# Optimization experiments

Measured on AMD Instinct MI355X. Metric: run time of the kernel, lower is better.

Reference implementation:

```python
import jax, jax.numpy as jnp
import numpy as np

# Dims: tokens [B,H,W,C]; 3x3 local window (NB=9 neighbors); relative-pos embed dim RP.
B, H, W, C = 4, 96, 96, 128
K, NB, RP = 3, 9, 8
HID = 128              # edge_hidden_dim = max(hidden_dim//2=128, feature_dim=128)
EDGE_IN = 3 * C + RP   # [center, neighbor, center-neighbor, rel_pos] -> 392
CLIP = 3.0
GATE_EPS = 1e-6
LN_EPS = 1e-5


def _ln(x, w, b):
    m = jnp.mean(x, axis=-1, keepdims=True)
    v = jnp.mean((x - m) ** 2, axis=-1, keepdims=True)
    return (x - m) * jax.lax.rsqrt(v + LN_EPS) * w + b


def _mlp(x, w1, b1, w2, b2):
    # Linear -> GELU (exact/erf, torch default) -> Linear; dropout is identity in eval mode.
    return jax.nn.gelu(x @ w1 + b1, approximate=False) @ w2 + b2


def _eml(drive, resistance, gamma_raw, lam, bias, warmup_eta):
    # EMLUnit energy gate (source not provided; Ohm's-law style drive/resistance,
    # positive resistance via softplus, clipped, warmup-scaled, learned bias).
    gamma = jax.nn.softplus(gamma_raw)
    conduct = drive / (jax.nn.softplus(resistance) + gamma + GATE_EPS)
    return warmup_eta * jnp.clip(lam * conduct, -CLIP, CLIP) + bias


def setup_inputs() -> dict:
    key = jax.random.key(0)
    ks = jax.random.split(key, 8)

    def w(k, shape, std=0.01):
        return jax.random.normal(k, shape, jnp.float32) * std

    return {
        "tokens": jax.random.normal(ks[0], (B, H, W, C), jnp.float32),
        "ln1_w": jnp.ones((C,), jnp.float32), "ln1_b": jnp.zeros((C,), jnp.float32),
        "ln2_w": jnp.ones((C,), jnp.float32), "ln2_b": jnp.zeros((C,), jnp.float32),
        "rel_pos": w(ks[1], (NB, RP), 0.02),
        "d_w1": w(ks[2], (EDGE_IN, HID)), "d_b1": jnp.zeros((HID,), jnp.float32),
        "d_w2": w(ks[3], (HID, 1)), "d_b2": jnp.zeros((1,), jnp.float32),
        "r_w1": w(ks[4], (EDGE_IN, HID)), "r_b1": jnp.zeros((HID,), jnp.float32),
        "r_w2": w(ks[5], (HID, 1)), "r_b2": jnp.zeros((1,), jnp.float32),
        "v_w": w(ks[6], (C, C)), "v_b": jnp.zeros((C,), jnp.float32),
        "o_w": w(ks[7], (C, C)), "o_b": jnp.zeros((C,), jnp.float32),
        "eml_gamma": jnp.full((1,), 0.1, jnp.float32),
        "eml_lam": jnp.ones((1,), jnp.float32),
        "eml_bias": jnp.full((1,), -0.3, jnp.float32),
    }


def reference(tokens, ln1_w, ln1_b, ln2_w, ln2_b, rel_pos,
              d_w1, d_b1, d_w2, d_b2, r_w1, r_b1, r_w2, r_b2,
              v_w, v_b, o_w, o_b, eml_gamma, eml_lam, eml_bias):
    b, h, w_, c = tokens.shape
    hw = h * w_
    norm = _ln(tokens, ln1_w, ln1_b)
    # nn.Unfold(kernel=3, padding=1): zero-pad then gather 3x3 windows (row-major ky,kx order).
    pad = jnp.pad(norm, ((0, 0), (1, 1), (1, 1), (0, 0)))
    neigh = jnp.stack([pad[:, dy:dy + h, dx:dx + w_, :]
                       for dy in range(K) for dx in range(K)], axis=3)  # [B,H,W,9,C]
    neigh = neigh.reshape(b, hw, NB, c)
    center = jnp.broadcast_to(norm.reshape(b, hw, 1, c), (b, hw, NB, c))
    relp = jnp.broadcast_to(rel_pos[None, None], (b, hw, NB, RP))
    edge = jnp.concatenate([center, neigh, center - neigh, relp], axis=-1)  # [B,HW,9,392]
    drive = _mlp(edge, d_w1, d_b1, d_w2, d_b2)[..., 0]        # [B,HW,9]
    resistance = _mlp(edge, r_w1, r_b1, r_w2, r_b2)[..., 0]   # [B,HW,9]
    energy = _eml(drive, resistance, eml_gamma, eml_lam, eml_bias, 1.0)
    gate = jax.nn.sigmoid(energy)[..., None]                  # [B,HW,9,1]
    values = neigh @ v_w + v_b                                # [B,HW,9,C]
    gate_mass = jnp.clip(jnp.sum(gate, axis=2), GATE_EPS, None)  # [B,HW,1]
    message = jnp.sum(gate * values, axis=2) / gate_mass      # [B,HW,C]
    update = (message @ o_w + o_b).reshape(b, h, w_, c)
    return _ln(tokens + update, ln2_w, ln2_b)
```

## Files before the change

### kernel.cpp

```cpp
#include <hip/hip_runtime.h>
#include <stdint.h>

#define NPIX 36864

using bf16x8 = __attribute__((ext_vector_type(8))) short;
using f32x4  = __attribute__((ext_vector_type(4))) float;
using f32x2  = __attribute__((ext_vector_type(2))) float;

__device__ __forceinline__ float bf2f(uint16_t u){
  return __uint_as_float(((uint32_t)u) << 16);
}
__device__ __forceinline__ float bl(uint32_t u){ return __uint_as_float(u << 16); }
__device__ __forceinline__ float bh(uint32_t u){ return __uint_as_float(u & 0xFFFF0000u); }
__device__ __forceinline__ uint16_t f2bf(float f){
  uint32_t u = __float_as_uint(f);
  u += 0x7fffu + ((u >> 16) & 1u);
  return (uint16_t)(u >> 16);
}
__device__ __forceinline__ float ldw(const void* p, int i, bool f32){
  return f32 ? ((const float*)p)[i] : bf2f(((const uint16_t*)p)[i]);
}
__device__ __forceinline__ bool probe_f32(const void* ones_vec){
  return ((const uint32_t*)ones_vec)[0] == 0x3F800000u;
}
__device__ __forceinline__ float softplusf(float x){
  return fmaxf(x, 0.f) + __logf(1.f + __expf(-fabsf(x)));
}
__device__ __forceinline__ f32x2 up2(uint32_t u){
  f32x2 r; r.x = __uint_as_float(u << 16); r.y = __uint_as_float(u & 0xFFFF0000u); return r;
}
__device__ __forceinline__ void sg2(f32x2& acc, uint32_t c, uint32_t n, f32x2 r, f32x2 w){
  f32x2 z = up2(c) + up2(n) + r;
  float sx = __builtin_amdgcn_fmed3f(fmaf(z.x, 0.4255f, 0.5f), 0.f, 1.f);
  float sy = __builtin_amdgcn_fmed3f(fmaf(z.y, 0.4255f, 0.5f), 0.f, 1.f);
  acc.x = fmaf(z.x * sx, w.x, acc.x);
  acc.y = fmaf(z.y * sy, w.y, acc.y);
}

#define LIDX(p, ch) ((p)*128 + ((((ch) >> 3) ^ ((p) & 15)) << 3) + ((ch) & 7))

__global__ __launch_bounds__(256) void pre_kernel(const void* __restrict__ tokens,
                            const void* __restrict__ ln1w, const void* __restrict__ ln1b,
                            const void* __restrict__ dw1, const void* __restrict__ rw1,
                            const void* __restrict__ vw,  const void* __restrict__ relp,
                            const void* __restrict__ db1, const void* __restrict__ rb1,
                            const void* __restrict__ ow,
                            const void* __restrict__ dw2, const void* __restrict__ rw2,
                            const void* __restrict__ vb,  const void* __restrict__ db2,
                            const void* __restrict__ rb2, const void* __restrict__ eg,
                            const void* __restrict__ el,  const void* __restrict__ eb,
                            uint16_t* __restrict__ norm,
                            uint16_t* __restrict__ wcatT, float* __restrict__ Rd,
                            float* __restrict__ Rr, uint16_t* __restrict__ owT,
                            float* __restrict__ w2df, float* __restrict__ w2rf,
                            float* __restrict__ vbf, float* __restrict__ sc){
  const bool F = probe_f32(ln1w);
  const int b = blockIdx.x;
  if (b < NPIX/4){
    const int wv = threadIdx.x >> 6, lane = threadIdx.x & 63;
    const int p = b * 4 + wv;
    float f0, f1;
    if (F){
      const float2 t = ((const float2*)tokens)[(size_t)p*64 + lane];
      f0 = t.x; f1 = t.y;
    } else {
      const uint32_t pk = ((const uint32_t*)tokens)[(size_t)p*64 + lane];
      f0 = bl(pk); f1 = bh(pk);
    }
    float s = f0 + f1;
    #pragma unroll
    for (int m = 1; m < 64; m <<= 1) s += __shfl_xor(s, m, 64);
    const float mean = s * (1.f/128.f);
    const float d0 = f0 - mean, d1 = f1 - mean;
    float q = d0*d0 + d1*d1;
    #pragma unroll
    for (int m = 1; m < 64; m <<= 1) q += __shfl_xor(q, m, 64);
    const float rs = rsqrtf(q * (1.f/128.f) + 1e-5f);
    const float n0 = d0*rs*ldw(ln1w, 2*lane, F)   + ldw(ln1b, 2*lane, F);
    const float n1 = d1*rs*ldw(ln1w, 2*lane+1, F) + ldw(ln1b, 2*lane+1, F);
    ((uint32_t*)(norm + (size_t)p*128))[lane] = (uint32_t)f2bf(n0) | ((uint32_t)f2bf(n1) << 16);
    return;
  }
  const int j = (b - NPIX/4) * 2 + (threadIdx.x >> 7);
  const int c = threadIdx.x & 127;
  if (j < 640){
    float val;
    if (j < 128)      val = ldw(dw1, c*128 + j, F)             + ldw(dw1, (256+c)*128 + j, F);
    else if (j < 256) val = ldw(dw1, (128+c)*128 + (j-128), F) - ldw(dw1, (256+c)*128 + (j-128), F);
    else if (j < 384) val = ldw(rw1, c*128 + (j-256), F)       + ldw(rw1, (256+c)*128 + (j-256), F);
    else if (j < 512) val = ldw(rw1, (128+c)*128 + (j-384), F) - ldw(rw1, (256+c)*128 + (j-384), F);
    else              val = ldw(vw, c*128 + (j-512), F);
    wcatT[j*128 + c] = f2bf(val);
  } else if (j < 649){
    const int k = j - 640;
    float sd = ldw(db1, c, F);
    float sr = ldw(rb1, c, F);
    #pragma unroll
    for (int r = 0; r < 8; ++r){
      float rp = ldw(relp, k*8 + r, F);
      sd += rp * ldw(dw1, (384+r)*128 + c, F);
      sr += rp * ldw(rw1, (384+r)*128 + c, F);
    }
    Rd[k*128 + c] = sd;
    Rr[k*128 + c] = sr;
  } else if (j < 777){
    const int n = j - 649;
    owT[n*128 + c] = f2bf(ldw(ow, c*128 + n, F));
  } else {
    w2df[c] = ldw(dw2, c, F);
    w2rf[c] = ldw(rw2, c, F);
    vbf[c]  = ldw(vb, c, F);
    if (c == 0){
      sc[0] = ldw(db2, 0, F);
      sc[1] = ldw(rb2, 0, F);
      sc[2] = softplusf(ldw(eg, 0, F));
      sc[3] = ldw(el, 0, F);
      sc[4] = ldw(eb, 0, F);
    }
  }
}

__global__ __launch_bounds__(256) void gemm1_kernel(const uint16_t* __restrict__ A,
                                                    const uint16_t* __restrict__ BT,
                                                    uint16_t* __restrict__ PT,
                                                    uint16_t* __restrict__ V){
  __shared__ __align__(16) char smem[49152];
  uint16_t* As = (uint16_t*)smem;
  uint16_t* Bs = (uint16_t*)(smem + 16384);
  const int row0 = blockIdx.x * 64;
  const int s    = blockIdx.y;
  const int t = threadIdx.x;
  #pragma unroll
  for (int i = 0; i < 4; ++i){
    const int cid = t + i*256;
    const int r = cid >> 4, c8 = cid & 15;
    *(uint4*)&As[r*128 + ((c8 ^ (r & 15)) << 3)] = *(const uint4*)&A[(size_t)(row0+r)*128 + c8*8];
  }
  #pragma unroll
  for (int i = 0; i < 8; ++i){
    const int cid = t + i*256;
    const int r = cid >> 4, c8 = cid & 15;
    *(uint4*)&Bs[r*128 + ((c8 ^ (r & 15)) << 3)] = *(const uint4*)&BT[(size_t)(s*128 + r)*128 + c8*8];
  }
  __syncthreads();
  const int wv = t >> 6, lane = t & 63;
  const int wc = wv * 32;
  const int lr = lane & 15, quad = lane >> 4;
  f32x4 acc[4][2] = {};
  #pragma unroll
  for (int kk = 0; kk < 4; ++kk){
    const int chunk = kk*4 + quad;
    bf16x8 a[4], b[2];
    #pragma unroll
    for (int mi = 0; mi < 4; ++mi){
      const int r = mi*16 + lr;
      a[mi] = *(const bf16x8*)&As[r*128 + ((chunk ^ (r & 15)) << 3)];
    }
    #pragma unroll
    for (int ni = 0; ni < 2; ++ni){
      const int r = wc + ni*16 + lr;
      b[ni] = *(const bf16x8*)&Bs[r*128 + ((chunk ^ (r & 15)) << 3)];
    }
    #pragma unroll
    for (int mi = 0; mi < 4; ++mi)
      #pragma unroll
      for (int ni = 0; ni < 2; ++ni)
        acc[mi][ni] = __builtin_amdgcn_mfma_f32_16x16x32_bf16(a[mi], b[ni], acc[mi][ni], 0, 0, 0);
  }
  __syncthreads();
  #pragma unroll
  for (int mi = 0; mi < 4; ++mi){
    #pragma unroll
    for (int ni = 0; ni < 2; ++ni){
      const int ch   = wc + ni*16 + lr;
      const int rowb = mi*16 + quad*4;
      #pragma unroll
      for (int r = 0; r < 4; ++r)
        As[LIDX(rowb + r, ch)] = f2bf(acc[mi][ni][r]);
    }
  }
  __syncthreads();
  if (s < 4){
    #pragma unroll
    for (int i = 0; i < 4; ++i){
      const int idx = t + i*256;
      const int p = idx & 63, c = idx >> 6;
      const uint4 v = *(const uint4*)&As[p*128 + ((c ^ (p & 15)) << 3)];
      ((uint4*)PT)[(size_t)(s*16 + c)*NPIX + (row0 + p)] = v;
    }
  } else {
    #pragma unroll
    for (int i = 0; i < 4; ++i){
      const int idx = t + i*256;
      const int c8 = idx & 15, p = idx >> 4;
      const uint4 v = *(const uint4*)&As[p*128 + ((c8 ^ (p & 15)) << 3)];
      ((uint4*)V)[(size_t)(row0 + p)*16 + c8] = v;
    }
  }
}

__global__ __launch_bounds__(64) void edge_kernel(const uint16_t* __restrict__ PTraw,
    const float* __restrict__ Rd, const float* __restrict__ Rr,
    const float* __restrict__ w2df, const float* __restrict__ w2rf,
    const float* __restrict__ sc, float* __restrict__ gates){
  const int lane = threadIdx.x;
  const int k = blockIdx.y;
  const int p = blockIdx.x * 64 + lane;
  const int dy = k/3 - 1, dx = k%3 - 1;
  const int x = p % 96, y = (p / 96) % 96;
  const bool inb = ((unsigned)(x + dx) < 96u) && ((unsigned)(y + dy) < 96u);
  const uint32_t m = inb ? 0xFFFFFFFFu : 0u;
  const int q = inb ? (p + dy*96 + dx) : p;
  const uint4* Cp = (const uint4*)PTraw + p;
  const uint4* Np = (const uint4*)PTraw + q;
  const float sc0 = sc[0], sc1 = sc[1], sc2 = sc[2], sc3 = sc[3], sc4 = sc[4];

  f32x2 ad = {0.f, 0.f};
  {
    const float4* r4 = (const float4*)(Rd + k*128);
    const float4* w4 = (const float4*)w2df;
    uint4 c = Cp[0];
    uint4 n = Np[(size_t)16*NPIX];
    #pragma unroll
    for (int i = 0; i < 16; ++i){
      uint4 cn, nn;
      if (i < 15){
        cn = Cp[(size_t)(i+1)*NPIX];
        nn = Np[(size_t)(16 + i+1)*NPIX];
      }
      n.x &= m; n.y &= m; n.z &= m; n.w &= m;
      const float4 rA = r4[2*i], rB = r4[2*i+1];
      const float4 wA = w4[2*i], wB = w4[2*i+1];
      sg2(ad, c.x, n.x, f32x2{rA.x, rA.y}, f32x2{wA.x, wA.y});
      sg2(ad, c.y, n.y, f32x2{rA.z, rA.w}, f32x2{wA.z, wA.w});
      sg2(ad, c.z, n.z, f32x2{rB.x, rB.y}, f32x2{wB.x, wB.y});
      sg2(ad, c.w, n.w, f32x2{rB.z, rB.w}, f32x2{wB.z, wB.w});
      c = cn; n = nn;
    }
  }
  f32x2 ar = {0.f, 0.f};
  {
    const float4* r4 = (const float4*)(Rr + k*128);
    const float4* w4 = (const float4*)w2rf;
    uint4 c = Cp[(size_t)32*NPIX];
    uint4 n = Np[(size_t)48*NPIX];
    #pragma unroll
    for (int i = 0; i < 16; ++i){
      uint4 cn, nn;
      if (i < 15){
        cn = Cp[(size_t)(32 + i+1)*NPIX];
        nn = Np[(size_t)(48 + i+1)*NPIX];
      }
      n.x &= m; n.y &= m; n.z &= m; n.w &= m;
      const float4 rA = r4[2*i], rB = r4[2*i+1];
      const float4 wA = w4[2*i], wB = w4[2*i+1];
      sg2(ar, c.x, n.x, f32x2{rA.x, rA.y}, f32x2{wA.x, wA.y});
      sg2(ar, c.y, n.y, f32x2{rA.z, rA.w}, f32x2{wA.z, wA.w});
      sg2(ar, c.z, n.z, f32x2{rB.x, rB.y}, f32x2{wB.x, wB.y});
      sg2(ar, c.w, n.w, f32x2{rB.z, rB.w}, f32x2{wB.z, wB.w});
      c = cn; n = nn;
    }
  }
  const float drive  = (ad.x + ad.y) + sc0;
  const float resist = (ar.x + ar.y) + sc1;
  const float cond = __fdividef(drive, softplusf(resist) + sc2 + 1e-6f);
  const float en = fminf(fmaxf(sc3 * cond, -3.0f), 3.0f) + sc4;
  const float e = __expf(-en);
  const float g = __builtin_amdgcn_rcpf(1.0f + e);
  gates[(size_t)k*NPIX + p] = g;
}

__global__ __launch_bounds__(256) void msg_kernel(const uint16_t* __restrict__ V,
    const float* __restrict__ gates, const float* __restrict__ vbf,
    uint16_t* __restrict__ msg){
  const int wv = __builtin_amdgcn_readfirstlane(threadIdx.x >> 6);
  const int lane = threadIdx.x & 63;
  const int p = blockIdx.x * 4 + wv;
  const int x = p % 96, y = (p / 96) % 96;
  float g[9], gsum = 0.f;
  #pragma unroll
  for (int k = 0; k < 9; ++k){ g[k] = gates[(size_t)k*NPIX + p]; gsum += g[k]; }
  float a0 = 0.f, a1 = 0.f;
  #pragma unroll
  for (int k = 0; k < 9; ++k){
    const int dy = k/3 - 1, dx = k%3 - 1;
    if (((unsigned)(y + dy) < 96u) && ((unsigned)(x + dx) < 96u)){
      const uint32_t u = ((const uint32_t*)(V + (size_t)(p + dy*96 + dx)*128))[lane];
      a0 = fmaf(g[k], bl(u), a0);
      a1 = fmaf(g[k], bh(u), a1);
    }
  }
  const float2 vb2 = ((const float2*)vbf)[lane];
  const float inv = __fdividef(1.0f, fmaxf(gsum, 1e-6f));
  a0 = (a0 + gsum * vb2.x) * inv;
  a1 = (a1 + gsum * vb2.y) * inv;
  ((uint32_t*)(msg + (size_t)p*128))[lane] = (uint32_t)f2bf(a0) | ((uint32_t)f2bf(a1) << 16);
}

__global__ __launch_bounds__(256) void out_kernel(const uint16_t* __restrict__ Amsg,
    const uint16_t* __restrict__ owT, const void* __restrict__ tokens,
    const void* __restrict__ ob,  const void* __restrict__ ln2w,
    const void* __restrict__ ln2b, void* __restrict__ out){
  const bool F = probe_f32(ln2w);
  __shared__ __align__(16) char smem[49152];
  uint16_t* Bs = (uint16_t*)smem;
  uint16_t* As = (uint16_t*)(smem + 32768);
  float*    U  = (float*)smem;
  const int row0 = blockIdx.x * 64;
  const int t = threadIdx.x;
  const int wv = t >> 6, lane = t & 63;
  #pragma unroll
  for (int i = 0; i < 8; ++i){
    const int cid = t + i*256;
    const int r = cid >> 4, c8 = cid & 15;
    *(uint4*)&Bs[r*128 + ((c8 ^ (r & 15)) << 3)] = *(const uint4*)&owT[(size_t)r*128 + c8*8];
  }
  #pragma unroll
  for (int i = 0; i < 4; ++i){
    const int cid = t + i*256;
    const int r = cid >> 4, c8 = cid & 15;
    *(uint4*)&As[r*128 + ((c8 ^ (r & 15)) << 3)] = *(const uint4*)&Amsg[(size_t)(row0+r)*128 + c8*8];
  }
  __syncthreads();
  const int wc = wv * 32;
  const int lr = lane & 15, quad = lane >> 4;
  f32x4 acc[4][2] = {};
  #pragma unroll
  for (int kk = 0; kk < 4; ++kk){
    const int chunk = kk*4 + quad;
    bf16x8 a[4], b[2];
    #pragma unroll
    for (int mi = 0; mi < 4; ++mi){
      const int r = mi*16 + lr;
      a[mi] = *(const bf16x8*)&As[r*128 + ((chunk ^ (r & 15)) << 3)];
    }
    #pragma unroll
    for (int ni = 0; ni < 2; ++ni){
      const int r = wc + ni*16 + lr;
      b[ni] = *(const bf16x8*)&Bs[r*128 + ((chunk ^ (r & 15)) << 3)];
    }
    #pragma unroll
    for (int mi = 0; mi < 4; ++mi)
      #pragma unroll
      for (int ni = 0; ni < 2; ++ni)
        acc[mi][ni] = __builtin_amdgcn_mfma_f32_16x16x32_bf16(a[mi], b[ni], acc[mi][ni], 0, 0, 0);
  }
  __syncthreads();
  #pragma unroll
  for (int mi = 0; mi < 4; ++mi)
    #pragma unroll
    for (int ni = 0; ni < 2; ++ni)
      #pragma unroll
      for (int r = 0; r < 4; ++r)
        U[(mi*16 + quad*4 + r)*128 + wc + ni*16 + lr] = acc[mi][ni][r];
  __syncthreads();
  const float lw0 = ldw(ln2w, 2*lane, F), lw1 = ldw(ln2w, 2*lane+1, F);
  const float lb0 = ldw(ln2b, 2*lane, F), lb1 = ldw(ln2b, 2*lane+1, F);
  const float ob0 = ldw(ob, 2*lane, F),   ob1 = ldw(ob, 2*lane+1, F);
  for (int j = 0; j < 16; ++j){
    const int row = wv*16 + j;
    const int p = row0 + row;
    const float2 uv = ((const float2*)U)[row*64 + lane];
    float t0, t1;
    if (F){
      const float2 tk = ((const float2*)tokens)[(size_t)p*64 + lane];
      t0 = tk.x; t1 = tk.y;
    } else {
      const uint32_t tk = ((const uint32_t*)tokens)[(size_t)p*64 + lane];
      t0 = bl(tk); t1 = bh(tk);
    }
    const float a0 = uv.x + ob0 + t0;
    const float a1 = uv.y + ob1 + t1;
    float s = a0 + a1;
    #pragma unroll
    for (int m = 1; m < 64; m <<= 1) s += __shfl_xor(s, m, 64);
    const float mean = s * (1.f/128.f);
    const float d0 = a0 - mean, d1 = a1 - mean;
    float q = d0*d0 + d1*d1;
    #pragma unroll
    for (int m = 1; m < 64; m <<= 1) q += __shfl_xor(q, m, 64);
    const float rs = rsqrtf(q * (1.f/128.f) + 1e-5f);
    const float o0 = d0*rs*lw0 + lb0;
    const float o1 = d1*rs*lw1 + lb1;
    if (F){
      ((float2*)out)[(size_t)p*64 + lane] = make_float2(o0, o1);
    } else {
      ((uint32_t*)out)[(size_t)p*64 + lane] = (uint32_t)f2bf(o0) | ((uint32_t)f2bf(o1) << 16);
    }
  }
}

extern "C" void kernel_launch(void* const* d_in, const int* in_sizes, int n_in,
                              void* d_out, int out_size, void* d_ws, size_t ws_size,
                              hipStream_t stream) {
  const void* tokens = d_in[0];
  const void* ln1w   = d_in[1];
  const void* ln1b   = d_in[2];
  const void* ln2w   = d_in[3];
  const void* ln2b   = d_in[4];
  const void* relp   = d_in[5];
  const void* dw1    = d_in[6];
  const void* db1    = d_in[7];
  const void* dw2    = d_in[8];
  const void* db2    = d_in[9];
  const void* rw1    = d_in[10];
  const void* rb1    = d_in[11];
  const void* rw2    = d_in[12];
  const void* rb2    = d_in[13];
  const void* vw     = d_in[14];
  const void* vb     = d_in[15];
  const void* ow     = d_in[16];
  const void* ob     = d_in[17];
  const void* eg     = d_in[18];
  const void* el     = d_in[19];
  const void* eb     = d_in[20];

  char* ws = (char*)d_ws;
  uint16_t* normb = (uint16_t*)(ws + 0);
  uint16_t* PT    = (uint16_t*)(ws + 9437184);
  uint16_t* V     = (uint16_t*)(ws + 47185920);
  float*    gates = (float*)   (ws + 56623104);
  uint16_t* wcatT = (uint16_t*)(ws + 57950208);
  float*    Rd    = (float*)   (ws + 58114048);
  float*    Rr    = (float*)   (ws + 58118656);
  uint16_t* owT   = (uint16_t*)(ws + 58123264);
  float*    w2df  = (float*)   (ws + 58156032);
  float*    w2rf  = (float*)   (ws + 58156544);
  float*    vbf   = (float*)   (ws + 58157056);
  float*    sc    = (float*)   (ws + 58157568);
  uint16_t* msg   = normb;

  pre_kernel<<<NPIX/4 + 389, 256, 0, stream>>>(tokens, ln1w, ln1b,
                                       dw1, rw1, vw, relp, db1, rb1, ow,
                                       dw2, rw2, vb, db2, rb2, eg, el, eb,
                                       normb, wcatT, Rd, Rr, owT, w2df, w2rf, vbf, sc);
  gemm1_kernel<<<dim3(NPIX/64, 5), 256, 0, stream>>>(normb, wcatT, PT, V);
  edge_kernel<<<dim3(NPIX/64, 9), 64, 0, stream>>>(PT, Rd, Rr, w2df, w2rf, sc, gates);
  msg_kernel<<<NPIX/4, 256, 0, stream>>>(V, gates, vbf, msg);
  out_kernel<<<NPIX/64, 256, 0, stream>>>(msg, owT, tokens, ob, ln2w, ln2b, d_out);
}
```

Measured before the change: 200.8 us.

## Fuse edge gating and message aggregation into one tiled kernel with LDS halo

Merges the edge and message kernels into a single kernel that works on 8x8 spatial tiles. Each block stages the neighbor projections and values, plus a one-pixel halo, in shared memory, so neighbor data is reused across the nine offsets instead of being re-read from global memory. Gates stay in LDS rather than going through a global buffer. The gemm1 output layout for PT changes from channel-major to pixel-major to suit this. The cost is a large LDS footprint (~79KB) with 576-thread blocks, which limits occupancy, and only 576 blocks are launched.

```diff
diff --git a/kernel.cpp b/kernel.cpp
--- a/kernel.cpp
+++ b/kernel.cpp
@@ -180,55 +180,87 @@
     }
   }
   __syncthreads();
-  if (s < 4){
-    #pragma unroll
-    for (int i = 0; i < 4; ++i){
-      const int idx = t + i*256;
-      const int p = idx & 63, c = idx >> 6;
-      const uint4 v = *(const uint4*)&As[p*128 + ((c ^ (p & 15)) << 3)];
-      ((uint4*)PT)[(size_t)(s*16 + c)*NPIX + (row0 + p)] = v;
-    }
-  } else {
-    #pragma unroll
-    for (int i = 0; i < 4; ++i){
-      const int idx = t + i*256;
-      const int c8 = idx & 15, p = idx >> 4;
-      const uint4 v = *(const uint4*)&As[p*128 + ((c8 ^ (p & 15)) << 3)];
-      ((uint4*)V)[(size_t)(row0 + p)*16 + c8] = v;
-    }
-  }
-}
-
-__global__ __launch_bounds__(64) void edge_kernel(const uint16_t* __restrict__ PTraw,
+  uint16_t* const dst = (s == 4) ? V : (PT + (size_t)s * NPIX * 128);
+  #pragma unroll
+  for (int i = 0; i < 4; ++i){
+    const int idx = t + i*256;
+    const int c8 = idx & 15, p = idx >> 4;
+    const uint4 v = *(const uint4*)&As[p*128 + ((c8 ^ (p & 15)) << 3)];
+    ((uint4*)dst)[(size_t)(row0 + p)*16 + c8] = v;
+  }
+}
+
+__global__ __launch_bounds__(576) void emsg_kernel(
+    const uint16_t* __restrict__ PT, const uint16_t* __restrict__ Vg,
     const float* __restrict__ Rd, const float* __restrict__ Rr,
     const float* __restrict__ w2df, const float* __restrict__ w2rf,
-    const float* __restrict__ sc, float* __restrict__ gates){
-  const int lane = threadIdx.x;
-  const int k = blockIdx.y;
-  const int p = blockIdx.x * 64 + lane;
-  const int dy = k/3 - 1, dx = k%3 - 1;
-  const int x = p % 96, y = (p / 96) % 96;
-  const bool inb = ((unsigned)(x + dx) < 96u) && ((unsigned)(y + dy) < 96u);
-  const uint32_t m = inb ? 0xFFFFFFFFu : 0u;
-  const int q = inb ? (p + dy*96 + dx) : p;
-  const uint4* Cp = (const uint4*)PTraw + p;
-  const uint4* Np = (const uint4*)PTraw + q;
+    const float* __restrict__ sc, const float* __restrict__ vbf,
+    uint16_t* __restrict__ msg){
+  __shared__ __align__(16) char smem[79104];
+  uint16_t* const PnD = (uint16_t*)smem;
+  uint16_t* const PnR = (uint16_t*)(smem + 25600);
+  uint16_t* const Vl  = (uint16_t*)(smem + 51200);
+  float*    const gl  = (float*)  (smem + 76800);
+
+  const int bid = blockIdx.x;
+  const int b   = bid / 144;
+  const int tl  = bid - b*144;
+  const int ty  = tl / 12;
+  const int y0  = ty * 8;
+  const int x0  = (tl - ty*12) * 8;
+  const int tid = threadIdx.x;
+
+  const uint16_t* const P1 = PT + (size_t)NPIX*128;
+  const uint16_t* const P3 = PT + (size_t)3*NPIX*128;
+
+  for (int i = tid; i < 4800; i += 576){
+    const int arr = i / 1600;
+    const int rem = i - arr*1600;
+    const int hq  = rem >> 4;
+    const int ch  = rem & 15;
+    const int hy  = hq / 10;
+    const int hx  = hq - hy*10;
+    const int y = y0 - 1 + hy, x = x0 - 1 + hx;
+    uint4 v = {0u, 0u, 0u, 0u};
+    if (((unsigned)y < 96u) && ((unsigned)x < 96u)){
+      const size_t pg = (size_t)((b*96 + y)*96 + x);
+      const uint16_t* src = (arr == 0 ? P1 : (arr == 1 ? P3 : Vg)) + pg*128 + ch*8;
+      v = *(const uint4*)src;
+    }
+    if (arr == 2){
+      *(uint4*)&Vl[hq*128 + ch*8] = v;
+    } else {
+      uint16_t* const d = (arr == 0) ? PnD : PnR;
+      *(uint4*)((char*)d + hq*256 + ((ch ^ (hq & 15)) << 4)) = v;
+    }
+  }
+  __syncthreads();
+
+  const int wv = tid >> 6, lane = tid & 63;
+  const int k  = __builtin_amdgcn_readfirstlane(wv);
+  const int ky = k / 3, kx = k - ky*3;
+  const int py = lane >> 3, px = lane & 7;
+  const int hq = (py + ky)*10 + (px + kx);
+  const size_t pg = (size_t)((b*96 + y0 + py)*96 + (x0 + px));
   const float sc0 = sc[0], sc1 = sc[1], sc2 = sc[2], sc3 = sc[3], sc4 = sc[4];
+  const char* const nbD = (const char*)PnD + hq*256;
+  const char* const nbR = (const char*)PnR + hq*256;
+  const int hsw = hq & 15;
 
   f32x2 ad = {0.f, 0.f};
   {
+    const uint4*  Cp = (const uint4*)(PT + pg*128);
     const float4* r4 = (const float4*)(Rd + k*128);
     const float4* w4 = (const float4*)w2df;
     uint4 c = Cp[0];
-    uint4 n = Np[(size_t)16*NPIX];
+    uint4 n = *(const uint4*)(nbD + ((0 ^ hsw) << 4));
     #pragma unroll
     for (int i = 0; i < 16; ++i){
       uint4 cn, nn;
       if (i < 15){
-        cn = Cp[(size_t)(i+1)*NPIX];
-        nn = Np[(size_t)(16 + i+1)*NPIX];
+        cn = Cp[i+1];
+        nn = *(const uint4*)(nbD + (((i+1) ^ hsw) << 4));
       }
-      n.x &= m; n.y &= m; n.z &= m; n.w &= m;
       const float4 rA = r4[2*i], rB = r4[2*i+1];
       const float4 wA = w4[2*i], wB = w4[2*i+1];
       sg2(ad, c.x, n.x, f32x2{rA.x, rA.y}, f32x2{wA.x, wA.y});
@@ -240,18 +272,18 @@
   }
   f32x2 ar = {0.f, 0.f};
   {
+    const uint4*  Cp = (const uint4*)(PT + (size_t)2*NPIX*128 + pg*128);
     const float4* r4 = (const float4*)(Rr + k*128);
     const float4* w4 = (const float4*)w2rf;
-    uint4 c = Cp[(size_t)32*NPIX];
-    uint4 n = Np[(size_t)48*NPIX];
+    uint4 c = Cp[0];
+    uint4 n = *(const uint4*)(nbR + ((0 ^ hsw) << 4));
     #pragma unroll
     for (int i = 0; i < 16; ++i){
       uint4 cn, nn;
       if (i < 15){
-        cn = Cp[(size_t)(32 + i+1)*NPIX];
-        nn = Np[(size_t)(48 + i+1)*NPIX];
+        cn = Cp[i+1];
+        nn = *(const uint4*)(nbR + (((i+1) ^ hsw) << 4));
       }
-      n.x &= m; n.y &= m; n.z &= m; n.w &= m;
       const float4 rA = r4[2*i], rB = r4[2*i+1];
       const float4 wA = w4[2*i], wB = w4[2*i+1];
       sg2(ar, c.x, n.x, f32x2{rA.x, rA.y}, f32x2{wA.x, wA.y});
@@ -266,35 +298,34 @@
   const float cond = __fdividef(drive, softplusf(resist) + sc2 + 1e-6f);
   const float en = fminf(fmaxf(sc3 * cond, -3.0f), 3.0f) + sc4;
   const float e = __expf(-en);
-  const float g = __builtin_amdgcn_rcpf(1.0f + e);
-  gates[(size_t)k*NPIX + p] = g;
-}
-
-__global__ __launch_bounds__(256) void msg_kernel(const uint16_t* __restrict__ V,
-    const float* __restrict__ gates, const float* __restrict__ vbf,
-    uint16_t* __restrict__ msg){
-  const int wv = __builtin_amdgcn_readfirstlane(threadIdx.x >> 6);
-  const int lane = threadIdx.x & 63;
-  const int p = blockIdx.x * 4 + wv;
-  const int x = p % 96, y = (p / 96) % 96;
-  float g[9], gsum = 0.f;
-  #pragma unroll
-  for (int k = 0; k < 9; ++k){ g[k] = gates[(size_t)k*NPIX + p]; gsum += g[k]; }
-  float a0 = 0.f, a1 = 0.f;
-  #pragma unroll
-  for (int k = 0; k < 9; ++k){
-    const int dy = k/3 - 1, dx = k%3 - 1;
-    if (((unsigned)(y + dy) < 96u) && ((unsigned)(x + dx) < 96u)){
-      const uint32_t u = ((const uint32_t*)(V + (size_t)(p + dy*96 + dx)*128))[lane];
-      a0 = fmaf(g[k], bl(u), a0);
-      a1 = fmaf(g[k], bh(u), a1);
-    }
-  }
-  const float2 vb2 = ((const float2*)vbf)[lane];
-  const float inv = __fdividef(1.0f, fmaxf(gsum, 1e-6f));
-  a0 = (a0 + gsum * vb2.x) * inv;
-  a1 = (a1 + gsum * vb2.y) * inv;
-  ((uint32_t*)(msg + (size_t)p*128))[lane] = (uint32_t)f2bf(a0) | ((uint32_t)f2bf(a1) << 16);
+  gl[k*64 + lane] = __builtin_amdgcn_rcpf(1.0f + e);
+  __syncthreads();
+
+  if (wv < 8){
+    const float2 vb2 = ((const float2*)vbf)[lane];
+    #pragma unroll
+    for (int j = 0; j < 8; ++j){
+      const int m  = wv*8 + j;
+      const int my = m >> 3, mx = m & 7;
+      float gk[9], gsum = 0.f;
+      #pragma unroll
+      for (int kk = 0; kk < 9; ++kk){ gk[kk] = gl[kk*64 + m]; gsum += gk[kk]; }
+      float a0 = 0.f, a1 = 0.f;
+      #pragma unroll
+      for (int kk = 0; kk < 9; ++kk){
+        const int kyy = kk / 3;
+        const int h2  = (my + kyy)*10 + (mx + kk - kyy*3);
+        const uint32_t u = ((const uint32_t*)Vl)[h2*64 + lane];
+        a0 = fmaf(gk[kk], bl(u), a0);
+        a1 = fmaf(gk[kk], bh(u), a1);
+      }
+      const float inv = __fdividef(1.0f, fmaxf(gsum, 1e-6f));
+      a0 = (a0 + gsum * vb2.x) * inv;
+      a1 = (a1 + gsum * vb2.y) * inv;
+      const size_t p2 = (size_t)((b*96 + y0 + my)*96 + (x0 + mx));
+      ((uint32_t*)msg)[p2*64 + lane] = (uint32_t)f2bf(a0) | ((uint32_t)f2bf(a1) << 16);
+    }
+  }
 }
 
 __global__ __launch_bounds__(256) void out_kernel(const uint16_t* __restrict__ Amsg,
@@ -419,7 +450,6 @@
   uint16_t* normb = (uint16_t*)(ws + 0);
   uint16_t* PT    = (uint16_t*)(ws + 9437184);
   uint16_t* V     = (uint16_t*)(ws + 47185920);
-  float*    gates = (float*)   (ws + 56623104);
   uint16_t* wcatT = (uint16_t*)(ws + 57950208);
   float*    Rd    = (float*)   (ws + 58114048);
   float*    Rr    = (float*)   (ws + 58118656);
@@ -435,7 +465,6 @@
                                        dw2, rw2, vb, db2, rb2, eg, el, eb,
                                        normb, wcatT, Rd, Rr, owT, w2df, w2rf, vbf, sc);
   gemm1_kernel<<<dim3(NPIX/64, 5), 256, 0, stream>>>(normb, wcatT, PT, V);
-  edge_kernel<<<dim3(NPIX/64, 9), 64, 0, stream>>>(PT, Rd, Rr, w2df, w2rf, sc, gates);
-  msg_kernel<<<NPIX/4, 256, 0, stream>>>(V, gates, vbf, msg);
+  emsg_kernel<<<576, 576, 0, stream>>>(PT, V, Rd, Rr, w2df, w2rf, sc, vbf, msg);
   out_kernel<<<NPIX/64, 256, 0, stream>>>(msg, owT, tokens, ob, ln2w, ln2b, d_out);
 }
```

Result: faster. 193.8 us (-3.5%).

## Fuse gemm, edge, message and output stages into one tiled mega kernel

Applied to the files above, without the earlier changes.

Replaces four kernels (projection GEMM, edge gating, gated message aggregation, output GEMM+LayerNorm) with one kernel per 8x8 spatial tile. Each tile stages a 10x10 halo of normalized tokens in LDS and recomputes the per-neighbor projections on that halo. Projections, gates and messages then stay in shared memory instead of round-tripping large intermediates (PT, V, gates, msg) through global memory. The cost is redundant halo GEMM work, heavy LDS usage (~108KB) limiting occupancy to one block per CU, many block-wide barriers, and only 576 blocks.

```diff
diff --git a/kernel.cpp b/kernel.cpp
--- a/kernel.cpp
+++ b/kernel.cpp
@@ -120,253 +120,239 @@
   }
 }
 
-__global__ __launch_bounds__(256) void gemm1_kernel(const uint16_t* __restrict__ A,
-                                                    const uint16_t* __restrict__ BT,
-                                                    uint16_t* __restrict__ PT,
-                                                    uint16_t* __restrict__ V){
-  __shared__ __align__(16) char smem[49152];
-  uint16_t* As = (uint16_t*)smem;
-  uint16_t* Bs = (uint16_t*)(smem + 16384);
-  const int row0 = blockIdx.x * 64;
-  const int s    = blockIdx.y;
-  const int t = threadIdx.x;
+__global__ __launch_bounds__(512) void mega_kernel(
+    const uint16_t* __restrict__ norm, const uint16_t* __restrict__ wcatT,
+    const uint16_t* __restrict__ owT,
+    const float* __restrict__ Rd, const float* __restrict__ Rr,
+    const float* __restrict__ w2df, const float* __restrict__ w2rf,
+    const float* __restrict__ sc, const float* __restrict__ vbf,
+    const void* __restrict__ tokens, const void* __restrict__ ob,
+    const void* __restrict__ ln2w, const void* __restrict__ ln2b,
+    void* __restrict__ out){
+  __shared__ __align__(16) char smem[111104];
+  uint16_t* const Ns = (uint16_t*)smem;
+  uint16_t* const PA = (uint16_t*)(smem + 28672);
+  uint16_t* const PB = (uint16_t*)(smem + 57344);
+  uint16_t* const Ws = (uint16_t*)(smem + 73728);
+  float*    const drv = (float*)(smem + 106496);
+  float*    const gts = (float*)(smem + 108800);
+  float*    const U   = (float*)smem;
+
+  const int bid0 = blockIdx.x;
+  const int bid  = (bid0 & 7)*72 + (bid0 >> 3);
+  const int b  = bid / 144;
+  const int tl = bid - b*144;
+  const int ty = tl / 12;
+  const int y0 = ty*8, x0 = (tl - ty*12)*8;
+  const int tid = threadIdx.x;
+  const int wv = tid >> 6, lane = tid & 63;
+  const int lr = lane & 15, quad = lane >> 4;
+  const float sc0 = sc[0], sc1 = sc[1], sc2 = sc[2], sc3 = sc[3], sc4 = sc[4];
+
   #pragma unroll
   for (int i = 0; i < 4; ++i){
-    const int cid = t + i*256;
-    const int r = cid >> 4, c8 = cid & 15;
-    *(uint4*)&As[r*128 + ((c8 ^ (r & 15)) << 3)] = *(const uint4*)&A[(size_t)(row0+r)*128 + c8*8];
-  }
-  #pragma unroll
-  for (int i = 0; i < 8; ++i){
-    const int cid = t + i*256;
-    const int r = cid >> 4, c8 = cid & 15;
-    *(uint4*)&Bs[r*128 + ((c8 ^ (r & 15)) << 3)] = *(const uint4*)&BT[(size_t)(s*128 + r)*128 + c8*8];
-  }
+    const int idx = tid + i*512;
+    if (idx < 1792){
+      const int hq = idx >> 4, g = idx & 15;
+      uint4 v = {0u,0u,0u,0u};
+      if (hq < 100){
+        const int hy = hq/10, hx = hq - hy*10;
+        const int y = y0 - 1 + hy, x = x0 - 1 + hx;
+        if (((unsigned)y < 96u) && ((unsigned)x < 96u))
+          v = *(const uint4*)&norm[((size_t)((b*96+y)*96+x))*128 + g*8];
+      }
+      *(uint4*)&Ns[hq*128 + ((g ^ (hq & 15)) << 3)] = v;
+    }
+  }
+
+  auto stageW = [&](const uint16_t* __restrict__ src){
+    #pragma unroll
+    for (int i = 0; i < 4; ++i){
+      const int idx = tid + i*512;
+      const int r = idx >> 4, g = idx & 15;
+      *(uint4*)&Ws[r*128 + ((g ^ (r & 15)) << 3)] = *(const uint4*)&src[(size_t)r*128 + g*8];
+    }
+  };
+
+  auto gemmH = [&](){
+    f32x4 acc[7] = {};
+    #pragma unroll
+    for (int kk = 0; kk < 4; ++kk){
+      const int chunk = kk*4 + quad;
+      const bf16x8 bf = *(const bf16x8*)&Ws[(wv*16+lr)*128 + ((chunk ^ lr) << 3)];
+      #pragma unroll
+      for (int mi = 0; mi < 7; ++mi){
+        const int r = mi*16 + lr;
+        const bf16x8 a = *(const bf16x8*)&Ns[r*128 + ((chunk ^ (r & 15)) << 3)];
+        acc[mi] = __builtin_amdgcn_mfma_f32_16x16x32_bf16(a, bf, acc[mi], 0, 0, 0);
+      }
+    }
+    const int col = wv*16 + lr;
+    #pragma unroll
+    for (int mi = 0; mi < 7; ++mi){
+      const int rowb = mi*16 + quad*4;
+      #pragma unroll
+      for (int r = 0; r < 4; ++r)
+        PA[LIDX(rowb + r, col)] = f2bf(acc[mi][r]);
+    }
+  };
+
+  auto gemmC = [&](){
+    f32x4 acc[4] = {};
+    #pragma unroll
+    for (int kk = 0; kk < 4; ++kk){
+      const int chunk = kk*4 + quad;
+      const bf16x8 bf = *(const bf16x8*)&Ws[(wv*16+lr)*128 + ((chunk ^ lr) << 3)];
+      #pragma unroll
+      for (int mi = 0; mi < 4; ++mi){
+        const int r = mi*16 + lr;
+        const int hr = (r >> 3)*10 + (r & 7) + 11;
+        const bf16x8 a = *(const bf16x8*)&Ns[hr*128 + ((chunk ^ (hr & 15)) << 3)];
+        acc[mi] = __builtin_amdgcn_mfma_f32_16x16x32_bf16(a, bf, acc[mi], 0, 0, 0);
+      }
+    }
+    const int col = wv*16 + lr;
+    #pragma unroll
+    for (int mi = 0; mi < 4; ++mi){
+      const int rowb = mi*16 + quad*4;
+      #pragma unroll
+      for (int r = 0; r < 4; ++r)
+        PB[LIDX(rowb + r, col)] = f2bf(acc[mi][r]);
+    }
+  };
+
+  auto edge = [&](const float* __restrict__ Rk, const float* __restrict__ w2, bool isDrive){
+    const int pl = lane >> 3, cg = lane & 7;
+    for (int i = 0; i < 9; ++i){
+      const int it = wv*9 + i;
+      const int k = it >> 3, ry = it & 7;
+      const int ky = k/3, kx = k - ky*3;
+      const int pr = ry*8 + pl;
+      const int hq = (ry + ky)*10 + pl + kx;
+      const int g0 = 2*cg;
+      const uint4 c0 = *(const uint4*)((const char*)PB + pr*256 + (((g0)  ^ (pr & 15)) << 4));
+      const uint4 c1 = *(const uint4*)((const char*)PB + pr*256 + (((g0+1)^ (pr & 15)) << 4));
+      const uint4 n0 = *(const uint4*)((const char*)PA + hq*256 + (((g0)  ^ (hq & 15)) << 4));
+      const uint4 n1 = *(const uint4*)((const char*)PA + hq*256 + (((g0+1)^ (hq & 15)) << 4));
+      const float4* r4 = (const float4*)(Rk + k*128) + cg*4;
+      const float4* w4 = (const float4*)w2 + cg*4;
+      const float4 Ra = r4[0], Rb = r4[1], Rc = r4[2], Rv = r4[3];
+      const float4 Wa = w4[0], Wb = w4[1], Wc = w4[2], Wd = w4[3];
+      f32x2 a = {0.f, 0.f};
+      sg2(a, c0.x, n0.x, f32x2{Ra.x, Ra.y}, f32x2{Wa.x, Wa.y});
+      sg2(a, c0.y, n0.y, f32x2{Ra.z, Ra.w}, f32x2{Wa.z, Wa.w});
+      sg2(a, c0.z, n0.z, f32x2{Rb.x, Rb.y}, f32x2{Wb.x, Wb.y});
+      sg2(a, c0.w, n0.w, f32x2{Rb.z, Rb.w}, f32x2{Wb.z, Wb.w});
+      sg2(a, c1.x, n1.x, f32x2{Rc.x, Rc.y}, f32x2{Wc.x, Wc.y});
+      sg2(a, c1.y, n1.y, f32x2{Rc.z, Rc.w}, f32x2{Wc.z, Wc.w});
+      sg2(a, c1.z, n1.z, f32x2{Rv.x, Rv.y}, f32x2{Wd.x, Wd.y});
+      sg2(a, c1.w, n1.w, f32x2{Rv.z, Rv.w}, f32x2{Wd.z, Wd.w});
+      float s = a.x + a.y;
+      s += __shfl_xor(s, 1, 64); s += __shfl_xor(s, 2, 64); s += __shfl_xor(s, 4, 64);
+      if (cg == 0){
+        if (isDrive){
+          drv[k*64 + pr] = s;
+        } else {
+          const float drive  = drv[k*64 + pr] + sc0;
+          const float resist = s + sc1;
+          const float cond = __fdividef(drive, softplusf(resist) + sc2 + 1e-6f);
+          const float en = fminf(fmaxf(sc3 * cond, -3.0f), 3.0f) + sc4;
+          const float e = __expf(-en);
+          gts[k*64 + pr] = __builtin_amdgcn_rcpf(1.0f + e);
+        }
+      }
+    }
+  };
+
+  const uint16_t* const W0 = wcatT;
+  const uint16_t* const W1 = wcatT + (size_t)1*128*128;
+  const uint16_t* const W2 = wcatT + (size_t)2*128*128;
+  const uint16_t* const W3 = wcatT + (size_t)3*128*128;
+  const uint16_t* const W4 = wcatT + (size_t)4*128*128;
+
+  stageW(W1); __syncthreads();
+  gemmH();    __syncthreads();
+  stageW(W0); __syncthreads();
+  gemmC();    __syncthreads();
+  stageW(W3);
+  edge(Rd, w2df, true);
   __syncthreads();
-  const int wv = t >> 6, lane = t & 63;
-  const int wc = wv * 32;
-  const int lr = lane & 15, quad = lane >> 4;
-  f32x4 acc[4][2] = {};
+  gemmH();    __syncthreads();
+  stageW(W2); __syncthreads();
+  gemmC();    __syncthreads();
+  stageW(W4);
+  edge(Rr, w2rf, false);
+  __syncthreads();
+  gemmH();    __syncthreads();
+  stageW(owT);
+
+  {
+    const float2 vb2 = ((const float2*)vbf)[lane];
+    const int g = lane >> 2, lb = (lane & 3)*4;
+    #pragma unroll
+    for (int j = 0; j < 8; ++j){
+      const int mp = wv*8 + j;
+      const int my = mp >> 3, mx = mp & 7;
+      float gk[9], gsum = 0.f;
+      #pragma unroll
+      for (int kk = 0; kk < 9; ++kk){ gk[kk] = gts[kk*64 + mp]; gsum += gk[kk]; }
+      float a0 = 0.f, a1 = 0.f;
+      #pragma unroll
+      for (int kk = 0; kk < 9; ++kk){
+        const int kyy = kk / 3;
+        const int h2  = (my + kyy)*10 + (mx + kk - kyy*3);
+        const uint32_t u = *(const uint32_t*)((const char*)PA + h2*256 + ((g ^ (h2 & 15)) << 4) + lb);
+        a0 = fmaf(gk[kk], bl(u), a0);
+        a1 = fmaf(gk[kk], bh(u), a1);
+      }
+      const float inv = __fdividef(1.0f, fmaxf(gsum, 1e-6f));
+      a0 = (a0 + gsum * vb2.x) * inv;
+      a1 = (a1 + gsum * vb2.y) * inv;
+      *(uint32_t*)((char*)PB + mp*256 + ((g ^ (mp & 15)) << 4) + lb) =
+          (uint32_t)f2bf(a0) | ((uint32_t)f2bf(a1) << 16);
+    }
+  }
+  __syncthreads();
+
+  f32x4 acc[4] = {};
   #pragma unroll
   for (int kk = 0; kk < 4; ++kk){
     const int chunk = kk*4 + quad;
-    bf16x8 a[4], b[2];
+    const bf16x8 bf = *(const bf16x8*)&Ws[(wv*16+lr)*128 + ((chunk ^ lr) << 3)];
     #pragma unroll
     for (int mi = 0; mi < 4; ++mi){
       const int r = mi*16 + lr;
-      a[mi] = *(const bf16x8*)&As[r*128 + ((chunk ^ (r & 15)) << 3)];
-    }
-    #pragma unroll
-    for (int ni = 0; ni < 2; ++ni){
-      const int r = wc + ni*16 + lr;
-      b[ni] = *(const bf16x8*)&Bs[r*128 + ((chunk ^ (r & 15)) << 3)];
-    }
+      const bf16x8 a = *(const bf16x8*)&PB[r*128 + ((chunk ^ (r & 15)) << 3)];
+      acc[mi] = __builtin_amdgcn_mfma_f32_16x16x32_bf16(a, bf, acc[mi], 0, 0, 0);
+    }
+  }
+  __syncthreads();
+  {
+    const int col = wv*16 + lr;
     #pragma unroll
     for (int mi = 0; mi < 4; ++mi)
       #pragma unroll
-      for (int ni = 0; ni < 2; ++ni)
-        acc[mi][ni] = __builtin_amdgcn_mfma_f32_16x16x32_bf16(a[mi], b[ni], acc[mi][ni], 0, 0, 0);
+      for (int r = 0; r < 4; ++r)
+        U[(mi*16 + quad*4 + r)*128 + col] = acc[mi][r];
   }
   __syncthreads();
-  #pragma unroll
-  for (int mi = 0; mi < 4; ++mi){
-    #pragma unroll
-    for (int ni = 0; ni < 2; ++ni){
-      const int ch   = wc + ni*16 + lr;
-      const int rowb = mi*16 + quad*4;
-      #pragma unroll
-      for (int r = 0; r < 4; ++r)
-        As[LIDX(rowb + r, ch)] = f2bf(acc[mi][ni][r]);
-    }
-  }
-  __syncthreads();
-  if (s < 4){
-    #pragma unroll
-    for (int i = 0; i < 4; ++i){
-      const int idx = t + i*256;
-      const int p = idx & 63, c = idx >> 6;
-      const uint4 v = *(const uint4*)&As[p*128 + ((c ^ (p & 15)) << 3)];
-      ((uint4*)PT)[(size_t)(s*16 + c)*NPIX + (row0 + p)] = v;
-    }
-  } else {
-    #pragma unroll
-    for (int i = 0; i < 4; ++i){
-      const int idx = t + i*256;
-      const int c8 = idx & 15, p = idx >> 4;
-      const uint4 v = *(const uint4*)&As[p*128 + ((c8 ^ (p & 15)) << 3)];
-      ((uint4*)V)[(size_t)(row0 + p)*16 + c8] = v;
-    }
-  }
-}
-
-__global__ __launch_bounds__(64) void edge_kernel(const uint16_t* __restrict__ PTraw,
-    const float* __restrict__ Rd, const float* __restrict__ Rr,
-    const float* __restrict__ w2df, const float* __restrict__ w2rf,
-    const float* __restrict__ sc, float* __restrict__ gates){
-  const int lane = threadIdx.x;
-  const int k = blockIdx.y;
-  const int p = blockIdx.x * 64 + lane;
-  const int dy = k/3 - 1, dx = k%3 - 1;
-  const int x = p % 96, y = (p / 96) % 96;
-  const bool inb = ((unsigned)(x + dx) < 96u) && ((unsigned)(y + dy) < 96u);
-  const uint32_t m = inb ? 0xFFFFFFFFu : 0u;
-  const int q = inb ? (p + dy*96 + dx) : p;
-  const uint4* Cp = (const uint4*)PTraw + p;
-  const uint4* Np = (const uint4*)PTraw + q;
-  const float sc0 = sc[0], sc1 = sc[1], sc2 = sc[2], sc3 = sc[3], sc4 = sc[4];
-
-  f32x2 ad = {0.f, 0.f};
-  {
-    const float4* r4 = (const float4*)(Rd + k*128);
-    const float4* w4 = (const float4*)w2df;
-    uint4 c = Cp[0];
-    uint4 n = Np[(size_t)16*NPIX];
-    #pragma unroll
-    for (int i = 0; i < 16; ++i){
-      uint4 cn, nn;
-      if (i < 15){
-        cn = Cp[(size_t)(i+1)*NPIX];
-        nn = Np[(size_t)(16 + i+1)*NPIX];
-      }
-      n.x &= m; n.y &= m; n.z &= m; n.w &= m;
-      const float4 rA = r4[2*i], rB = r4[2*i+1];
-      const float4 wA = w4[2*i], wB = w4[2*i+1];
-      sg2(ad, c.x, n.x, f32x2{rA.x, rA.y}, f32x2{wA.x, wA.y});
-      sg2(ad, c.y, n.y, f32x2{rA.z, rA.w}, f32x2{wA.z, wA.w});
-      sg2(ad, c.z, n.z, f32x2{rB.x, rB.y}, f32x2{wB.x, wB.y});
-      sg2(ad, c.w, n.w, f32x2{rB.z, rB.w}, f32x2{wB.z, wB.w});
-      c = cn; n = nn;
-    }
-  }
-  f32x2 ar = {0.f, 0.f};
-  {
-    const float4* r4 = (const float4*)(Rr + k*128);
-    const float4* w4 = (const float4*)w2rf;
-    uint4 c = Cp[(size_t)32*NPIX];
-    uint4 n = Np[(size_t)48*NPIX];
-    #pragma unroll
-    for (int i = 0; i < 16; ++i){
-      uint4 cn, nn;
-      if (i < 15){
-        cn = Cp[(size_t)(32 + i+1)*NPIX];
-        nn = Np[(size_t)(48 + i+1)*NPIX];
-      }
-      n.x &= m; n.y &= m; n.z &= m; n.w &= m;
-      const float4 rA = r4[2*i], rB = r4[2*i+1];
-      const float4 wA = w4[2*i], wB = w4[2*i+1];
-      sg2(ar, c.x, n.x, f32x2{rA.x, rA.y}, f32x2{wA.x, wA.y});
-      sg2(ar, c.y, n.y, f32x2{rA.z, rA.w}, f32x2{wA.z, wA.w});
-      sg2(ar, c.z, n.z, f32x2{rB.x, rB.y}, f32x2{wB.x, wB.y});
-      sg2(ar, c.w, n.w, f32x2{rB.z, rB.w}, f32x2{wB.z, wB.w});
-      c = cn; n = nn;
-    }
-  }
-  const float drive  = (ad.x + ad.y) + sc0;
-  const float resist = (ar.x + ar.y) + sc1;
-  const float cond = __fdividef(drive, softplusf(resist) + sc2 + 1e-6f);
-  const float en = fminf(fmaxf(sc3 * cond, -3.0f), 3.0f) + sc4;
-  const float e = __expf(-en);
-  const float g = __builtin_amdgcn_rcpf(1.0f + e);
-  gates[(size_t)k*NPIX + p] = g;
-}
-
-__global__ __launch_bounds__(256) void msg_kernel(const uint16_t* __restrict__ V,
-    const float* __restrict__ gates, const float* __restrict__ vbf,
-    uint16_t* __restrict__ msg){
-  const int wv = __builtin_amdgcn_readfirstlane(threadIdx.x >> 6);
-  const int lane = threadIdx.x & 63;
-  const int p = blockIdx.x * 4 + wv;
-  const int x = p % 96, y = (p / 96) % 96;
-  float g[9], gsum = 0.f;
-  #pragma unroll
-  for (int k = 0; k < 9; ++k){ g[k] = gates[(size_t)k*NPIX + p]; gsum += g[k]; }
-  float a0 = 0.f, a1 = 0.f;
-  #pragma unroll
-  for (int k = 0; k < 9; ++k){
-    const int dy = k/3 - 1, dx = k%3 - 1;
-    if (((unsigned)(y + dy) < 96u) && ((unsigned)(x + dx) < 96u)){
-      const uint32_t u = ((const uint32_t*)(V + (size_t)(p + dy*96 + dx)*128))[lane];
-      a0 = fmaf(g[k], bl(u), a0);
-      a1 = fmaf(g[k], bh(u), a1);
-    }
-  }
-  const float2 vb2 = ((const float2*)vbf)[lane];
-  const float inv = __fdividef(1.0f, fmaxf(gsum, 1e-6f));
-  a0 = (a0 + gsum * vb2.x) * inv;
-  a1 = (a1 + gsum * vb2.y) * inv;
-  ((uint32_t*)(msg + (size_t)p*128))[lane] = (uint32_t)f2bf(a0) | ((uint32_t)f2bf(a1) << 16);
-}
-
-__global__ __launch_bounds__(256) void out_kernel(const uint16_t* __restrict__ Amsg,
-    const uint16_t* __restrict__ owT, const void* __restrict__ tokens,
-    const void* __restrict__ ob,  const void* __restrict__ ln2w,
-    const void* __restrict__ ln2b, void* __restrict__ out){
+
   const bool F = probe_f32(ln2w);
-  __shared__ __align__(16) char smem[49152];
-  uint16_t* Bs = (uint16_t*)smem;
-  uint16_t* As = (uint16_t*)(smem + 32768);
-  float*    U  = (float*)smem;
-  const int row0 = blockIdx.x * 64;
-  const int t = threadIdx.x;
-  const int wv = t >> 6, lane = t & 63;
-  #pragma unroll
-  for (int i = 0; i < 8; ++i){
-    const int cid = t + i*256;
-    const int r = cid >> 4, c8 = cid & 15;
-    *(uint4*)&Bs[r*128 + ((c8 ^ (r & 15)) << 3)] = *(const uint4*)&owT[(size_t)r*128 + c8*8];
-  }
-  #pragma unroll
-  for (int i = 0; i < 4; ++i){
-    const int cid = t + i*256;
-    const int r = cid >> 4, c8 = cid & 15;
-    *(uint4*)&As[r*128 + ((c8 ^ (r & 15)) << 3)] = *(const uint4*)&Amsg[(size_t)(row0+r)*128 + c8*8];
-  }
-  __syncthreads();
-  const int wc = wv * 32;
-  const int lr = lane & 15, quad = lane >> 4;
-  f32x4 acc[4][2] = {};
-  #pragma unroll
-  for (int kk = 0; kk < 4; ++kk){
-    const int chunk = kk*4 + quad;
-    bf16x8 a[4], b[2];
-    #pragma unroll
-    for (int mi = 0; mi < 4; ++mi){
-      const int r = mi*16 + lr;
-      a[mi] = *(const bf16x8*)&As[r*128 + ((chunk ^ (r & 15)) << 3)];
-    }
-    #pragma unroll
-    for (int ni = 0; ni < 2; ++ni){
-      const int r = wc + ni*16 + lr;
-      b[ni] = *(const bf16x8*)&Bs[r*128 + ((chunk ^ (r & 15)) << 3)];
-    }
-    #pragma unroll
-    for (int mi = 0; mi < 4; ++mi)
-      #pragma unroll
-      for (int ni = 0; ni < 2; ++ni)
-        acc[mi][ni] = __builtin_amdgcn_mfma_f32_16x16x32_bf16(a[mi], b[ni], acc[mi][ni], 0, 0, 0);
-  }
-  __syncthreads();
-  #pragma unroll
-  for (int mi = 0; mi < 4; ++mi)
-    #pragma unroll
-    for (int ni = 0; ni < 2; ++ni)
-      #pragma unroll
-      for (int r = 0; r < 4; ++r)
-        U[(mi*16 + quad*4 + r)*128 + wc + ni*16 + lr] = acc[mi][ni][r];
-  __syncthreads();
   const float lw0 = ldw(ln2w, 2*lane, F), lw1 = ldw(ln2w, 2*lane+1, F);
   const float lb0 = ldw(ln2b, 2*lane, F), lb1 = ldw(ln2b, 2*lane+1, F);
   const float ob0 = ldw(ob, 2*lane, F),   ob1 = ldw(ob, 2*lane+1, F);
-  for (int j = 0; j < 16; ++j){
-    const int row = wv*16 + j;
-    const int p = row0 + row;
+  #pragma unroll
+  for (int j = 0; j < 8; ++j){
+    const int row = wv*8 + j;
+    const int my = row >> 3, mx = row & 7;
+    const size_t p = (size_t)((b*96 + y0 + my)*96 + (x0 + mx));
     const float2 uv = ((const float2*)U)[row*64 + lane];
     float t0, t1;
     if (F){
-      const float2 tk = ((const float2*)tokens)[(size_t)p*64 + lane];
+      const float2 tk = ((const float2*)tokens)[p*64 + lane];
       t0 = tk.x; t1 = tk.y;
     } else {
-      const uint32_t tk = ((const uint32_t*)tokens)[(size_t)p*64 + lane];
+      const uint32_t tk = ((const uint32_t*)tokens)[p*64 + lane];
       t0 = bl(tk); t1 = bh(tk);
     }
     const float a0 = uv.x + ob0 + t0;
@@ -383,9 +369,9 @@
     const float o0 = d0*rs*lw0 + lb0;
     const float o1 = d1*rs*lw1 + lb1;
     if (F){
-      ((float2*)out)[(size_t)p*64 + lane] = make_float2(o0, o1);
+      ((float2*)out)[p*64 + lane] = make_float2(o0, o1);
     } else {
-      ((uint32_t*)out)[(size_t)p*64 + lane] = (uint32_t)f2bf(o0) | ((uint32_t)f2bf(o1) << 16);
+      ((uint32_t*)out)[p*64 + lane] = (uint32_t)f2bf(o0) | ((uint32_t)f2bf(o1) << 16);
     }
   }
 }
@@ -417,25 +403,19 @@
 
   char* ws = (char*)d_ws;
   uint16_t* normb = (uint16_t*)(ws + 0);
-  uint16_t* PT    = (uint16_t*)(ws + 9437184);
-  uint16_t* V     = (uint16_t*)(ws + 47185920);
-  float*    gates = (float*)   (ws + 56623104);
-  uint16_t* wcatT = (uint16_t*)(ws + 57950208);
-  float*    Rd    = (float*)   (ws + 58114048);
-  float*    Rr    = (float*)   (ws + 58118656);
-  uint16_t* owT   = (uint16_t*)(ws + 58123264);
-  float*    w2df  = (float*)   (ws + 58156032);
-  float*    w2rf  = (float*)   (ws + 58156544);
-  float*    vbf   = (float*)   (ws + 58157056);
-  float*    sc    = (float*)   (ws + 58157568);
-  uint16_t* msg   = normb;
+  uint16_t* wcatT = (uint16_t*)(ws + 9437184);
+  float*    Rd    = (float*)   (ws + 9601024);
+  float*    Rr    = (float*)   (ws + 9605632);
+  uint16_t* owT   = (uint16_t*)(ws + 9610240);
+  float*    w2df  = (float*)   (ws + 9643008);
+  float*    w2rf  = (float*)   (ws + 9643520);
+  float*    vbf   = (float*)   (ws + 9644032);
+  float*    sc    = (float*)   (ws + 9644544);
 
   pre_kernel<<<NPIX/4 + 389, 256, 0, stream>>>(tokens, ln1w, ln1b,
                                        dw1, rw1, vw, relp, db1, rb1, ow,
                                        dw2, rw2, vb, db2, rb2, eg, el, eb,
                                        normb, wcatT, Rd, Rr, owT, w2df, w2rf, vbf, sc);
-  gemm1_kernel<<<dim3(NPIX/64, 5), 256, 0, stream>>>(normb, wcatT, PT, V);
-  edge_kernel<<<dim3(NPIX/64, 9), 64, 0, stream>>>(PT, Rd, Rr, w2df, w2rf, sc, gates);
-  msg_kernel<<<NPIX/4, 256, 0, stream>>>(V, gates, vbf, msg);
-  out_kernel<<<NPIX/64, 256, 0, stream>>>(msg, owT, tokens, ob, ln2w, ln2b, d_out);
-}
+  mega_kernel<<<576, 512, 0, stream>>>(normb, wcatT, owT, Rd, Rr, w2df, w2rf,
+                                       sc, vbf, tokens, ob, ln2w, ln2b, d_out);
+}
```

Result: no change. 204.3 us (+1.8%).
